# Optimization experiments

Measured on AMD Instinct MI355X. Metric: run time of the kernel, lower is better.

The kernel has to match this reference:

```python
import jax, jax.numpy as jnp
from jax import lax
import numpy as np

NBINS = 50

def _make_filters():
    coords = np.linspace(-1.0, 1.0, 3)
    zz, yy, xx = np.meshgrid(coords, coords, coords, indexing='ij')
    gf = []
    for freq in [2.0, 4.0]:
        for ang in [0.0, np.pi / 4, np.pi / 2, 3 * np.pi / 4]:
            gauss = np.exp(-(xx ** 2 + yy ** 2 + zz ** 2) / 0.5)
            f = gauss * np.cos(freq * (xx * np.cos(ang) + yy * np.sin(ang)))
            f = f - f.mean()
            s = f.std(ddof=1)  # torch std is unbiased
            if s > 1e-8:
                f = f / s
            gf.append(f)
    gf = np.stack(gf)[:, None].astype(np.float32)  # (8,1,3,3,3)
    lf = []
    for axis in range(3):
        for sign in [1, -1]:
            f = np.zeros((3, 3, 3), np.float32)
            f[1, 1, 1] = 1.0
            idx = [1, 1, 1]
            idx[axis] += sign
            f[tuple(idx)] = -1.0
            lf.append(f)
    lf = np.stack(lf)[:, None].astype(np.float32)  # (6,1,3,3,3)
    return gf, lf

def setup_inputs() -> dict:
    key = jax.random.key(0)
    k1, k2 = jax.random.split(key)
    B, D, H, W = 4, 96, 160, 160
    x = jax.random.uniform(k1, (B, 1, D, H, W), jnp.float32, minval=-1.0, maxval=1.0)
    mask = (jax.random.uniform(k2, (B, 1, D, H, W), jnp.float32) > 0.5).astype(jnp.float32)
    gf, lf = _make_filters()
    return {"x": x, "mask": mask, "gabor_filters": jnp.asarray(gf), "lbp_filters": jnp.asarray(lf)}

def _hu_stats(v, mf):
    # v, mf: (B,D,H,W); mf is 0/1 float mask
    n = mf.sum((1, 2, 3))                      # (B,)
    nn = jnp.maximum(n, 1.0)
    mu = (mf * v).sum((1, 2, 3)) / nn
    diff = (v - mu[:, None, None, None]) * mf
    var = (diff ** 2).sum((1, 2, 3)) / jnp.maximum(n - 1.0, 1.0)  # unbiased, like torch .std()
    sigma = jnp.sqrt(var) + 1e-8
    z = diff / sigma[:, None, None, None]
    skew = (z ** 3).sum((1, 2, 3)) / nn
    kurt = (z ** 4).sum((1, 2, 3)) / nn - 3.0
    # histogram over [-1,1] with 50 bins; torch.histc ignores out-of-range, last bin inclusive
    w = mf * ((v >= -1.0) & (v <= 1.0)).astype(v.dtype)
    idx = jnp.clip(jnp.floor((v + 1.0) * (NBINS / 2.0)).astype(jnp.int32), 0, NBINS - 1)
    hist = jax.vmap(lambda i, wb: jnp.zeros((NBINS,), v.dtype).at[i.ravel()].add(wb.ravel()))(idx, w)
    p = hist / (hist.sum(-1, keepdims=True) + 1e-8)
    ent = -(p * jnp.log(p + 1e-8)).sum(-1)
    valid = (n >= 10.0).astype(v.dtype)
    return jnp.stack([mu, sigma, skew, kurt, ent], axis=1) * valid[:, None]  # (B,5)

def _glcm_proxy(v, m):
    # v: (B,D,H,W) float; m: (B,D,H,W) bool
    rows = []
    for axis in range(3):
        a = axis + 1
        sl1 = tuple(slice(None, -1) if i == a else slice(None) for i in range(4))
        sl2 = tuple(slice(1, None) if i == a else slice(None) for i in range(4))
        d = v[sl1] - v[sl2]
        mp = (m[sl1] & m[sl2]).astype(v.dtype)
        s = mp.sum((1, 2, 3))
        ss = jnp.maximum(s, 1.0)
        con = (mp * d * d).sum((1, 2, 3)) / ss
        hom = (mp / (1.0 + d * d)).sum((1, 2, 3)) / ss
        ok = (s >= 4.0).astype(v.dtype)
        rows += [con * ok, hom * ok]
    return jnp.stack(rows, axis=1)  # (B,6)

def _forward(x, mask, gabor_filters, lbp_filters):
    v = x[:, 0]                       # (B,D,H,W)
    m = mask[:, 0] > 0.5              # bool
    mf = m.astype(x.dtype)
    hu = _hu_stats(v, mf)             # (B,5)
    dn = ('NCDHW', 'OIDHW', 'NCDHW')
    pad = [(1, 1)] * 3
    gab = lax.conv_general_dilated(x, gabor_filters, (1, 1, 1), pad, dimension_numbers=dn)
    lung_vol = jnp.clip(mask.sum((2, 3, 4)), 1.0, None)      # (B,1)
    gab_feat = jnp.abs(gab * mask).sum((2, 3, 4)) / lung_vol  # (B,8)
    lbp = lax.conv_general_dilated(x, lbp_filters, (1, 1, 1), pad, dimension_numbers=dn)
    lbp = lbp * mask
    lbp_feat = ((lbp > 0).astype(x.dtype) * mask).sum((2, 3, 4)) / lung_vol  # (B,6)
    glcm = _glcm_proxy(v, m)          # (B,6)
    return jnp.concatenate([hu, gab_feat, lbp_feat, glcm], axis=1)  # (B,25)

def reference(x, mask, gabor_filters, lbp_filters):
    return _forward(x, mask, gabor_filters, lbp_filters)
```

## Files before the change

kernel.cpp:

```cpp
#include <hip/hip_runtime.h>
#include <math.h>

#define B_    4
#define D_    96
#define H_    160
#define W_    160
#define HW_   (H_ * W_)
#define NVOX  (D_ * H_ * W_)
#define NBINS 50
#define NQR   28
#define CPB   256
#define PART_F (B_ * NQR * CPB)
#define HIST_U PART_F
#define WQ_F   (PART_F + 200)
#define LASTP ((D_ - 1) * HW_)

typedef float f2 __attribute__((ext_vector_type(2)));

__device__ __forceinline__ float rfl(float v) {
    return __uint_as_float(__builtin_amdgcn_readfirstlane(__float_as_uint(v)));
}

__global__ __launch_bounds__(64) void radiomics_weights(
    const float* __restrict__ gf, const float* __restrict__ lf,
    float* __restrict__ ws)
{
    const int lane = threadIdx.x;
    __shared__ float sCs[8][5], sR[8], sMO[8], sMC[8];
    if (lane < 8) {
        const int f = lane;
        float O9[9], C9[9];
        float mC = 0.f, mO = 0.f;
#pragma unroll
        for (int k = 0; k < 9; ++k) {
            O9[k] = gf[f * 27 + k];
            C9[k] = gf[f * 27 + 9 + k];
            mC += C9[k]; mO += O9[k];
        }
        mC *= (1.f / 9.f); mO *= (1.f / 9.f);
        float cov = 0.f, var = 0.f;
#pragma unroll
        for (int k = 0; k < 9; ++k) {
            float c = C9[k] - mC, o = O9[k] - mO;
            cov += c * o; var += c * c;
        }
        sR[f] = cov / var; sMO[f] = mO; sMC[f] = mC;
#pragma unroll
        for (int j = 0; j < 4; ++j) sCs[f][j] = 0.5f * (C9[j] + C9[8 - j]);
        sCs[f][4] = C9[4];
    }
    __syncthreads();
    if (lane == 0) {
        float* wq = ws + WQ_F;
        float gz0 = 0.f;
        for (int f = 0; f < 8; ++f) gz0 += sR[f];
        gz0 *= 0.125f;
        wq[0] = gz0;
        float df[8];
        for (int f = 0; f < 8; ++f) df[f] = sMO[f] - gz0 * sMC[f];
        for (int F = 0; F < 2; ++F) {
            const int f0 = 4 * F, f1 = 4 * F + 1, f2 = 4 * F + 2, f3 = 4 * F + 3;
            float* g = wq + 1 + 11 * F;
            g[0]  = 0.5f * (df[f0] + df[f2]);
            g[1]  = 0.5f * (sCs[f0][0] + sCs[f2][0]);
            g[2]  = 0.5f * (sCs[f0][2] + sCs[f2][2]);
            g[3]  = 0.5f * (sCs[f0][4] + sCs[f2][4]);
            g[4]  = 0.5f * (sCs[f0][1] + sCs[f2][3]);
            g[5]  = 0.5f * (sCs[f0][3] + sCs[f2][1]);
            g[6]  = 0.5f * (df[f1] + df[f3]);
            g[7]  = 0.25f * (sCs[f1][1] + sCs[f1][3]
                           + sCs[f3][1] + sCs[f3][3]);
            g[8]  = 0.5f * (sCs[f1][4] + sCs[f3][4]);
            g[9]  = 0.5f * (sCs[f1][0] + sCs[f3][2]);
            g[10] = 0.5f * (sCs[f1][2] + sCs[f3][0]);
        }
    }
    unsigned int* gh = (unsigned int*)ws + HIST_U;
    for (int i = lane; i < B_ * NBINS; i += 64) gh[i] = 0u;
}

#define LOADP(s, zo) do {                                                   \
    _Pragma("unroll")                                                       \
    for (int r_ = 0; r_ < 3; ++r_) {                                        \
        Xw[s][r_][0] = xbb[(zo) + rowoff[r_] + xL];                         \
        f2 t_ = *(const f2*)(xbb + (zo) + rowoff[r_] + gx);                 \
        Xw[s][r_][1] = t_.x; Xw[s][r_][2] = t_.y;                           \
        Xw[s][r_][3] = xbb[(zo) + rowoff[r_] + xR];                         \
    }                                                                       \
} while (0)

#define FINISH(s, bzv) do {                                                 \
    if ((bzv) == 0.f) {                                                     \
        _Pragma("unroll")                                                   \
        for (int r_ = 0; r_ < 3; ++r_)                                      \
            _Pragma("unroll")                                               \
            for (int c_ = 0; c_ < 4; ++c_) Xw[s][r_][c_] = 0.f;             \
        S9[s][0] = S9[s][1] = 0.f;                                          \
    } else {                                                                \
        _Pragma("unroll")                                                   \
        for (int c_ = 0; c_ < 4; ++c_) {                                    \
            Xw[s][0][c_] *= bndRow0; Xw[s][2][c_] *= bndRow2;               \
        }                                                                   \
        _Pragma("unroll")                                                   \
        for (int r_ = 0; r_ < 3; ++r_) {                                    \
            Xw[s][r_][0] *= bndL; Xw[s][r_][3] *= bndR;                     \
        }                                                                   \
        float cs0_ = Xw[s][0][0] + Xw[s][1][0] + Xw[s][2][0];               \
        float cs1_ = Xw[s][0][1] + Xw[s][1][1] + Xw[s][2][1];               \
        float cs2_ = Xw[s][0][2] + Xw[s][1][2] + Xw[s][2][2];               \
        float cs3_ = Xw[s][0][3] + Xw[s][1][3] + Xw[s][2][3];               \
        S9[s][0] = cs0_ + cs1_ + cs2_;                                      \
        S9[s][1] = cs1_ + cs2_ + cs3_;                                      \
    }                                                                       \
} while (0)

__global__ __launch_bounds__(256) void radiomics_main(
    const float* __restrict__ x, const float* __restrict__ mask,
    float* __restrict__ ws)
{
    __shared__ unsigned int shist[4 * NBINS];
    __shared__ float xred[4][NQR];

    const int tid = threadIdx.x;
    const int tx = tid & 15, ty = tid >> 4;
    const int lane = tid & 63, wid = tid >> 6;

    for (int i = tid; i < 4 * NBINS; i += 256) shist[i] = 0u;

    const float* wq = ws + WQ_F;
    const float gz0 = rfl(wq[0]);
    float gco[22];
#pragma unroll
    for (int i = 0; i < 22; ++i) gco[i] = rfl(wq[1 + i]);

    const int c = blockIdx.x;
    const int b = blockIdx.z;
    int t, z0, nz;
    if (c < 36) {
        t  = c / 6;
        const int ci = c - 6 * t;
        z0 = 16 * ci; nz = 16;
    } else {
        const int c2i = c - 36;
        const int ti = c2i / 5;
        const int ci = c2i - 5 * ti;
        t = 6 + ti;
        if (ci == 0) { z0 = 0; nz = 16; }
        else         { z0 = 20 * ci - 4; nz = 20; }
    }
    const int ngroups = nz >> 2;

    const int gx = (t % 5) * 32 + tx * 2;
    const int gy = (t / 5) * 16 + ty;

    const float* __restrict__ xbb = x    + (size_t)b * NVOX;
    const float* __restrict__ mbb = mask + (size_t)b * NVOX;

    const int gy0 = (gy > 0) ? gy - 1 : 0;
    const int gy2 = (gy + 1 < H_) ? gy + 1 : H_ - 1;
    const int rowoff[3] = { gy0 * W_, gy * W_, gy2 * W_ };
    const float bndRow0 = (gy > 0) ? 1.f : 0.f;
    const float bndRow2 = (gy + 1 < H_) ? 1.f : 0.f;
    const int xL = (gx > 0) ? gx - 1 : 0;
    const int xR = (gx + 2 < W_) ? gx + 2 : W_ - 1;
    const float bndL = (gx > 0) ? 1.f : 0.f;
    const float bndR = (gx + 2 < W_) ? 1.f : 0.f;
    const int moff  = gy * W_ + gx;
    const int myoff = gy2 * W_ + gx;
    const int mxoff = gy * W_ + xR;
    const float bym = bndRow2, bxm = bndR;

    float Xw[4][3][4];
    float S9[4][2];
    float Mq[4][2];
    float bzs[4];
    f2    myq[2];
    float mxq[2];
    float acc[NQR];
#pragma unroll
    for (int q = 0; q < NQR; ++q) acc[q] = 0.f;
    bzs[0] = bzs[1] = bzs[2] = 1.f;

    if (z0 == 0) {
#pragma unroll
        for (int r = 0; r < 3; ++r)
#pragma unroll
            for (int cc = 0; cc < 4; ++cc) Xw[0][r][cc] = 0.f;
        S9[0][0] = S9[0][1] = 0.f;
    } else {
        LOADP(0, (z0 - 1) * HW_);
        FINISH(0, 1.f);
    }
    LOADP(1, z0 * HW_);
    FINISH(1, 1.f);
    {
        f2 mm = *(const f2*)(mbb + z0 * HW_ + moff);
        Mq[1][0] = (mm.x > 0.5f) ? 1.f : 0.f;
        Mq[1][1] = (mm.y > 0.5f) ? 1.f : 0.f;
    }
    LOADP(2, (z0 + 1) * HW_);
    {
        f2 mm = *(const f2*)(mbb + (z0 + 1) * HW_ + moff);
        Mq[2][0] = mm.x; Mq[2][1] = mm.y;
    }
    Mq[0][0] = Mq[0][1] = 0.f;
    myq[0] = *(const f2*)(mbb + z0 * HW_ + myoff);
    mxq[0] = mbb[z0 * HW_ + mxoff];

    int zc   = z0 * HW_;
    int zpre = (z0 + 2) * HW_;

#pragma unroll 1
    for (int g = 0; g < ngroups; ++g) {
#pragma unroll
        for (int j = 0; j < 4; ++j) {
            const int c0 = j & 3;
            const int cs = (j + 1) & 3;
            const int c2 = (j + 2) & 3;
            const int c3 = (j + 3) & 3;
            const int cur = j & 1, nxt = cur ^ 1;

            const int zpe = (zpre < NVOX) ? zpre : LASTP;
            bzs[c3] = (zpre < NVOX) ? 1.f : 0.f;
            LOADP(c3, zpe);
            {
                f2 mm = *(const f2*)(mbb + zpe + moff);
                Mq[c3][0] = mm.x; Mq[c3][1] = mm.y;
            }
            const int zn = (zc + HW_ < NVOX) ? zc + HW_ : LASTP;
            myq[nxt] = *(const f2*)(mbb + zn + myoff);
            mxq[nxt] = mbb[zn + mxoff];

            const f2 my2 = myq[cur];
            const float mxs = mxq[cur];

#pragma unroll
            for (int q = 0; q < 2; ++q) {
                const float v  = Xw[cs][1][q + 1];
                const float mc = Mq[cs][q];

                acc[0] += mc;
                float mv  = mc * v;  acc[1] += mv;
                float mv2 = mv * v;  acc[2] += mv2;
                float mv3 = mv2 * v; acc[3] += mv3;
                acc[4] += mv3 * v;

                if (mc > 0.5f && v >= -1.f && v <= 1.f) {
                    int bi = (int)((v + 1.f) * (NBINS * 0.5f));
                    bi = min(bi, NBINS - 1);
                    atomicAdd(&shist[(tid >> 6) * NBINS + bi], 1u);
                }

                acc[14] += (v > Xw[c0][1][q + 1]) ? mc : 0.f;
                acc[15] += (v > Xw[cs][2][q + 1]) ? mc : 0.f;
                acc[16] += (v > Xw[cs][0][q + 1]) ? mc : 0.f;
                acc[17] += (v > Xw[cs][1][q + 2]) ? mc : 0.f;
                acc[18] += (v > Xw[cs][1][q])     ? mc : 0.f;

                {
                    float mr = (q == 0) ? my2.x : my2.y;
                    float mp = mc * (((mr > 0.5f) ? 1.f : 0.f) * bym);
                    float d = v - Xw[cs][2][q + 1], dd = d * d;
                    acc[20] += mp;
                    acc[23] = fmaf(mp, dd, acc[23]);
                    acc[26] = fmaf(mp, __builtin_amdgcn_rcpf(1.f + dd), acc[26]);
                }
                {
                    float mnr = (q == 0) ? Mq[cs][1] : (((mxs > 0.5f) ? 1.f : 0.f) * bxm);
                    float mp = mc * mnr;
                    float d = v - Xw[cs][1][q + 2], dd = d * d;
                    acc[21] += mp;
                    acc[24] = fmaf(mp, dd, acc[24]);
                    acc[27] = fmaf(mp, __builtin_amdgcn_rcpf(1.f + dd), acc[27]);
                }
            }

            FINISH(c2, bzs[c2]);
            Mq[c2][0] = (Mq[c2][0] * bzs[c2] > 0.5f) ? 1.f : 0.f;
            Mq[c2][1] = (Mq[c2][1] * bzs[c2] > 0.5f) ? 1.f : 0.f;

            float T6[3][4];
#pragma unroll
            for (int r = 0; r < 3; ++r)
#pragma unroll
                for (int cc = 0; cc < 4; ++cc)
                    T6[r][cc] = fmaf(gz0, Xw[c0][r][cc] + Xw[c2][r][cc], Xw[cs][r][cc]);

#pragma unroll
            for (int q = 0; q < 2; ++q) {
                const float v  = Xw[cs][1][q + 1];
                const float mc = Mq[cs][q];

                float P0 = T6[0][q]     + T6[2][q + 2];
                float P1 = T6[0][q + 1] + T6[2][q + 1];
                float P2 = T6[0][q + 2] + T6[2][q];
                float P3 = T6[1][q]     + T6[1][q + 2];
                float ctrv = T6[1][q + 1];
                float S2 = S9[c0][q] + S9[c2][q];
                float Qv = P1 + P3;
#pragma unroll
                for (int F = 0; F < 2; ++F) {
                    const float dfA = gco[F*11+0], c0s = gco[F*11+1];
                    const float c2s = gco[F*11+2], c4s = gco[F*11+3];
                    const float cu  = gco[F*11+4], cw  = gco[F*11+5];
                    const float dfB = gco[F*11+6], ct  = gco[F*11+7];
                    const float ce  = gco[F*11+8], ca  = gco[F*11+9];
                    const float cb  = gco[F*11+10];
                    float E = dfA * S2;
                    E = fmaf(c0s, P0, E); E = fmaf(c2s, P2, E); E = fmaf(c4s, ctrv, E);
                    float r0   = fmaf(cu, P1, fmaf(cw, P3, E));
                    float r90  = fmaf(cw, P1, fmaf(cu, P3, E));
                    float G = fmaf(ct, Qv, dfB * S2);
                    G = fmaf(ce, ctrv, G);
                    float r45  = fmaf(ca, P0, fmaf(cb, P2, G));
                    float r135 = fmaf(cb, P0, fmaf(ca, P2, G));
                    acc[5 + 4*F + 0] = fmaf(fabsf(r0),   mc, acc[5 + 4*F + 0]);
                    acc[5 + 4*F + 1] = fmaf(fabsf(r45),  mc, acc[5 + 4*F + 1]);
                    acc[5 + 4*F + 2] = fmaf(fabsf(r90),  mc, acc[5 + 4*F + 2]);
                    acc[5 + 4*F + 3] = fmaf(fabsf(r135), mc, acc[5 + 4*F + 3]);
                }

                acc[13] += (v > Xw[c2][1][q + 1]) ? mc : 0.f;

                {
                    float mp = mc * Mq[c2][q];
                    float d = v - Xw[c2][1][q + 1], dd = d * d;
                    acc[19] += mp;
                    acc[22] = fmaf(mp, dd, acc[22]);
                    acc[25] = fmaf(mp, __builtin_amdgcn_rcpf(1.f + dd), acc[25]);
                }
            }
            zc += HW_; zpre += HW_;
        }
    }

#pragma unroll
    for (int q = 0; q < NQR; ++q) {
        float sm = acc[q];
#pragma unroll
        for (int o = 32; o > 0; o >>= 1)
            sm += __shfl_down(sm, o, 64);
        acc[q] = sm;
    }
    if (lane == 0) {
#pragma unroll
        for (int q = 0; q < NQR; ++q) xred[wid][q] = acc[q];
    }
    __syncthreads();

    if (tid < NQR) {
        float v = xred[0][tid] + xred[1][tid] + xred[2][tid] + xred[3][tid];
        ws[((size_t)b * NQR + tid) * CPB + c] = v;
    } else if (tid < NQR + NBINS) {
        int h = tid - NQR;
        unsigned int cnt = shist[h] + shist[NBINS + h]
                         + shist[2 * NBINS + h] + shist[3 * NBINS + h];
        unsigned int* ghist = (unsigned int*)ws + HIST_U;
        if (cnt) atomicAdd(&ghist[b * NBINS + h], cnt);
    }
}

__global__ __launch_bounds__(512) void radiomics_tail(
    const float* __restrict__ ws, float* __restrict__ out)
{
    __shared__ double fin[NQR];
    __shared__ double hcnt[NBINS];
    __shared__ double entp[NBINS];
    __shared__ double sh_hsum;
    const int b = blockIdx.x, tid = threadIdx.x;
    const int wave = tid >> 6, lane = tid & 63;

    for (int q = wave; q < NQR; q += 8) {
        const float* p = ws + ((size_t)b * NQR + q) * CPB;
        double s = 0.0;
#pragma unroll
        for (int k = 0; k < 4; ++k)
            s += (double)p[lane + 64 * k];
#pragma unroll
        for (int o = 32; o > 0; o >>= 1)
            s += __shfl_down(s, o, 64);
        if (lane == 0) fin[q] = s;
    }
    if (tid < NBINS)
        hcnt[tid] = (double)(((const unsigned int*)ws)[HIST_U + b * NBINS + tid]);
    __syncthreads();

    if (tid == 0) {
        double h = 0.0;
        for (int k = 0; k < NBINS; ++k) h += hcnt[k];
        sh_hsum = h + 1e-8;
    }
    __syncthreads();

    if (tid < NBINS) {
        double p = hcnt[tid] / sh_hsum;
        entp[tid] = -p * log(p + 1e-8);
    }
    __syncthreads();

    if (tid == 0) {
        const double n  = fin[0];
        const double nn = fmax(n, 1.0);
        const double s1 = fin[1], s2 = fin[2], s3 = fin[3], s4 = fin[4];
        const double mu = s1 / nn;
        const double M2 = s2 - 2.0 * mu * s1 + mu * mu * n;
        const double M3 = s3 - 3.0 * mu * s2 + 3.0 * mu * mu * s1 - mu * mu * mu * n;
        const double M4 = s4 - 4.0 * mu * s3 + 6.0 * mu * mu * s2
                          - 4.0 * mu * mu * mu * s1 + mu * mu * mu * mu * n;
        const double var   = M2 / fmax(n - 1.0, 1.0);
        const double sigma = sqrt(var) + 1e-8;
        const double skew  = M3 / (sigma * sigma * sigma) / nn;
        const double kurt  = M4 / (sigma * sigma * sigma * sigma) / nn - 3.0;

        double ent = 0.0;
        for (int k = 0; k < NBINS; ++k) ent += entp[k];

        const double valid = (n >= 10.0) ? 1.0 : 0.0;
        float* ob = out + b * 25;
        ob[0] = (float)(mu * valid);
        ob[1] = (float)(sigma * valid);
        ob[2] = (float)(skew * valid);
        ob[3] = (float)(kurt * valid);
        ob[4] = (float)(ent * valid);

        const double lung = fmax(n, 1.0);
        for (int f = 0; f < 8; ++f) ob[5 + f]  = (float)(fin[5 + f] / lung);
        for (int f = 0; f < 6; ++f) ob[13 + f] = (float)(fin[13 + f] / lung);

        for (int ax = 0; ax < 3; ++ax) {
            double s  = fin[19 + ax];
            double ss = fmax(s, 1.0);
            double ok = (s >= 4.0) ? 1.0 : 0.0;
            ob[19 + 2 * ax]     = (float)(fin[22 + ax] / ss * ok);
            ob[19 + 2 * ax + 1] = (float)(fin[25 + ax] / ss * ok);
        }
    }
}

extern "C" void kernel_launch(void* const* d_in, const int* in_sizes, int n_in,
                              void* d_out, int out_size, void* d_ws, size_t ws_size,
                              hipStream_t stream)
{
    const float* x    = (const float*)d_in[0];
    const float* mask = (const float*)d_in[1];
    const float* gf   = (const float*)d_in[2];
    const float* lf   = (const float*)d_in[3];
    float* out = (float*)d_out;
    float* ws  = (float*)d_ws;

    radiomics_weights<<<1, 64, 0, stream>>>(gf, lf, ws);
    radiomics_main<<<dim3(256, 1, B_), 256, 0, stream>>>(x, mask, ws);
    radiomics_tail<<<B_, 512, 0, stream>>>(ws, out);
}
```

Baseline: 165.4 us.

## Share y-neighbour rows via wave shuffles and rebalance z-chunk partition

Each thread now loads only its centre row plus one halo row (top row in a wave for the upper halo, bottom row for the lower), and gets the other y-neighbours from adjacent lanes with __shfl_up/__shfl_down by 16. This cuts global loads per slice from three rows to two and shrinks register arrays. The z-slicing is also redone so the grid has 320 blocks per batch with a different chunk split, and the tail reduction is widened to match. The cost is extra shuffle instructions and select logic.

```diff
diff --git a/kernel.cpp b/kernel.cpp
--- a/kernel.cpp
+++ b/kernel.cpp
@@ -9,7 +9,7 @@
 #define NVOX  (D_ * H_ * W_)
 #define NBINS 50
 #define NQR   28
-#define CPB   256
+#define CPB   320
 #define PART_F (B_ * NQR * CPB)
 #define HIST_U PART_F
 #define WQ_F   (PART_F + 200)
@@ -79,38 +79,35 @@
     for (int i = lane; i < B_ * NBINS; i += 64) gh[i] = 0u;
 }
 
-#define LOADP(s, zo) do {                                                   \
-    _Pragma("unroll")                                                       \
-    for (int r_ = 0; r_ < 3; ++r_) {                                        \
-        Xw[s][r_][0] = xbb[(zo) + rowoff[r_] + xL];                         \
-        f2 t_ = *(const f2*)(xbb + (zo) + rowoff[r_] + gx);                 \
-        Xw[s][r_][1] = t_.x; Xw[s][r_][2] = t_.y;                           \
-        Xw[s][r_][3] = xbb[(zo) + rowoff[r_] + xR];                         \
-    }                                                                       \
+#define LOADR(s, zo) do {                                                   \
+    Xc[s][0] = xbb[(zo) + rowC + xL];                                       \
+    f2 t_ = *(const f2*)(xbb + (zo) + rowC + gx);                           \
+    Xc[s][1] = t_.x; Xc[s][2] = t_.y;                                       \
+    Xc[s][3] = xbb[(zo) + rowC + xR];                                       \
+    hal[s][0] = xbb[(zo) + rowH + xL];                                      \
+    f2 h_ = *(const f2*)(xbb + (zo) + rowH + gx);                           \
+    hal[s][1] = h_.x; hal[s][2] = h_.y;                                     \
+    hal[s][3] = xbb[(zo) + rowH + xR];                                      \
 } while (0)
 
 #define FINISH(s, bzv) do {                                                 \
     if ((bzv) == 0.f) {                                                     \
-        _Pragma("unroll")                                                   \
-        for (int r_ = 0; r_ < 3; ++r_)                                      \
-            _Pragma("unroll")                                               \
-            for (int c_ = 0; c_ < 4; ++c_) Xw[s][r_][c_] = 0.f;             \
+        Xc[s][0] = Xc[s][1] = Xc[s][2] = Xc[s][3] = 0.f;                    \
+        hal[s][0] = hal[s][1] = hal[s][2] = hal[s][3] = 0.f;                \
         S9[s][0] = S9[s][1] = 0.f;                                          \
     } else {                                                                \
-        _Pragma("unroll")                                                   \
-        for (int c_ = 0; c_ < 4; ++c_) {                                    \
-            Xw[s][0][c_] *= bndRow0; Xw[s][2][c_] *= bndRow2;               \
-        }                                                                   \
-        _Pragma("unroll")                                                   \
-        for (int r_ = 0; r_ < 3; ++r_) {                                    \
-            Xw[s][r_][0] *= bndL; Xw[s][r_][3] *= bndR;                     \
-        }                                                                   \
-        float cs0_ = Xw[s][0][0] + Xw[s][1][0] + Xw[s][2][0];               \
-        float cs1_ = Xw[s][0][1] + Xw[s][1][1] + Xw[s][2][1];               \
-        float cs2_ = Xw[s][0][2] + Xw[s][1][2] + Xw[s][2][2];               \
-        float cs3_ = Xw[s][0][3] + Xw[s][1][3] + Xw[s][2][3];               \
-        S9[s][0] = cs0_ + cs1_ + cs2_;                                      \
-        S9[s][1] = cs1_ + cs2_ + cs3_;                                      \
+        Xc[s][0] *= bndL; Xc[s][3] *= bndR;                                 \
+        hal[s][0] *= bndL; hal[s][3] *= bndR;                               \
+        float rs0_ = Xc[s][0] + Xc[s][1] + Xc[s][2];                        \
+        float rs1_ = Xc[s][1] + Xc[s][2] + Xc[s][3];                        \
+        float hrs0_ = hal[s][0] + hal[s][1] + hal[s][2];                    \
+        float hrs1_ = hal[s][1] + hal[s][2] + hal[s][3];                    \
+        float u0_ = __shfl_up(rs0_, 16, 64), d0_ = __shfl_down(rs0_, 16, 64); \
+        float u1_ = __shfl_up(rs1_, 16, 64), d1_ = __shfl_down(rs1_, 16, 64); \
+        S9[s][0] = (isTop ? hrs0_ : u0_) * bndRow0 + rs0_                   \
+                 + (isBot ? hrs0_ : d0_) * bndRow2;                         \
+        S9[s][1] = (isTop ? hrs1_ : u1_) * bndRow0 + rs1_                   \
+                 + (isBot ? hrs1_ : d1_) * bndRow2;                         \
     }                                                                       \
 } while (0)
 
@@ -123,7 +120,10 @@
 
     const int tid = threadIdx.x;
     const int tx = tid & 15, ty = tid >> 4;
+    const int tyw = ty & 3;
     const int lane = tid & 63, wid = tid >> 6;
+    const bool isTop = (tyw == 0);
+    const bool isBot = (tyw == 3);
 
     for (int i = tid; i < 4 * NBINS; i += 256) shist[i] = 0u;
 
@@ -136,17 +136,17 @@
     const int c = blockIdx.x;
     const int b = blockIdx.z;
     int t, z0, nz;
-    if (c < 36) {
-        t  = c / 6;
-        const int ci = c - 6 * t;
+    if (c < 140) {
+        t = c / 7;
+        const int ci = c - 7 * t;
+        if (ci < 3) { z0 = 16 * ci; nz = 16; }
+        else        { z0 = 48 + 12 * (ci - 3); nz = 12; }
+    } else {
+        const int c2i = c - 140;
+        const int ti = c2i / 6;
+        const int ci = c2i - 6 * ti;
+        t = 20 + ti;
         z0 = 16 * ci; nz = 16;
-    } else {
-        const int c2i = c - 36;
-        const int ti = c2i / 5;
-        const int ci = c2i - 5 * ti;
-        t = 6 + ti;
-        if (ci == 0) { z0 = 0; nz = 16; }
-        else         { z0 = 20 * ci - 4; nz = 20; }
     }
     const int ngroups = nz >> 2;
 
@@ -158,7 +158,8 @@
 
     const int gy0 = (gy > 0) ? gy - 1 : 0;
     const int gy2 = (gy + 1 < H_) ? gy + 1 : H_ - 1;
-    const int rowoff[3] = { gy0 * W_, gy * W_, gy2 * W_ };
+    const int rowC = gy * W_;
+    const int rowH = (isBot ? gy2 : gy0) * W_;
     const float bndRow0 = (gy > 0) ? 1.f : 0.f;
     const float bndRow2 = (gy + 1 < H_) ? 1.f : 0.f;
     const int xL = (gx > 0) ? gx - 1 : 0;
@@ -170,35 +171,32 @@
     const int mxoff = gy * W_ + xR;
     const float bym = bndRow2, bxm = bndR;
 
-    float Xw[4][3][4];
+    float Xc[4][4];
+    float hal[4][4];
     float S9[4][2];
     float Mq[4][2];
-    float bzs[4];
     f2    myq[2];
     float mxq[2];
     float acc[NQR];
 #pragma unroll
     for (int q = 0; q < NQR; ++q) acc[q] = 0.f;
-    bzs[0] = bzs[1] = bzs[2] = 1.f;
 
     if (z0 == 0) {
 #pragma unroll
-        for (int r = 0; r < 3; ++r)
-#pragma unroll
-            for (int cc = 0; cc < 4; ++cc) Xw[0][r][cc] = 0.f;
+        for (int cc = 0; cc < 4; ++cc) { Xc[0][cc] = 0.f; hal[0][cc] = 0.f; }
         S9[0][0] = S9[0][1] = 0.f;
     } else {
-        LOADP(0, (z0 - 1) * HW_);
+        LOADR(0, (z0 - 1) * HW_);
         FINISH(0, 1.f);
     }
-    LOADP(1, z0 * HW_);
+    LOADR(1, z0 * HW_);
     FINISH(1, 1.f);
     {
         f2 mm = *(const f2*)(mbb + z0 * HW_ + moff);
         Mq[1][0] = (mm.x > 0.5f) ? 1.f : 0.f;
         Mq[1][1] = (mm.y > 0.5f) ? 1.f : 0.f;
     }
-    LOADP(2, (z0 + 1) * HW_);
+    LOADR(2, (z0 + 1) * HW_);
     {
         f2 mm = *(const f2*)(mbb + (z0 + 1) * HW_ + moff);
         Mq[2][0] = mm.x; Mq[2][1] = mm.y;
@@ -207,6 +205,7 @@
     myq[0] = *(const f2*)(mbb + z0 * HW_ + myoff);
     mxq[0] = mbb[z0 * HW_ + mxoff];
 
+    int z    = z0;
     int zc   = z0 * HW_;
     int zpre = (z0 + 2) * HW_;
 
@@ -221,8 +220,7 @@
             const int cur = j & 1, nxt = cur ^ 1;
 
             const int zpe = (zpre < NVOX) ? zpre : LASTP;
-            bzs[c3] = (zpre < NVOX) ? 1.f : 0.f;
-            LOADP(c3, zpe);
+            LOADR(c3, zpe);
             {
                 f2 mm = *(const f2*)(mbb + zpe + moff);
                 Mq[c3][0] = mm.x; Mq[c3][1] = mm.y;
@@ -234,9 +232,18 @@
             const f2 my2 = myq[cur];
             const float mxs = mxq[cur];
 
+            float yup[2], ydn[2];
 #pragma unroll
             for (int q = 0; q < 2; ++q) {
-                const float v  = Xw[cs][1][q + 1];
+                float up = __shfl_up(Xc[cs][q + 1], 16, 64);
+                float dn = __shfl_down(Xc[cs][q + 1], 16, 64);
+                yup[q] = (isTop ? hal[cs][q + 1] : up) * bndRow0;
+                ydn[q] = (isBot ? hal[cs][q + 1] : dn) * bndRow2;
+            }
+
+#pragma unroll
+            for (int q = 0; q < 2; ++q) {
+                const float v  = Xc[cs][q + 1];
                 const float mc = Mq[cs][q];
 
                 acc[0] += mc;
@@ -251,16 +258,16 @@
                     atomicAdd(&shist[(tid >> 6) * NBINS + bi], 1u);
                 }
 
-                acc[14] += (v > Xw[c0][1][q + 1]) ? mc : 0.f;
-                acc[15] += (v > Xw[cs][2][q + 1]) ? mc : 0.f;
-                acc[16] += (v > Xw[cs][0][q + 1]) ? mc : 0.f;
-                acc[17] += (v > Xw[cs][1][q + 2]) ? mc : 0.f;
-                acc[18] += (v > Xw[cs][1][q])     ? mc : 0.f;
+                acc[14] += (v > Xc[c0][q + 1]) ? mc : 0.f;
+                acc[15] += (v > ydn[q])        ? mc : 0.f;
+                acc[16] += (v > yup[q])        ? mc : 0.f;
+                acc[17] += (v > Xc[cs][q + 2]) ? mc : 0.f;
+                acc[18] += (v > Xc[cs][q])     ? mc : 0.f;
 
                 {
                     float mr = (q == 0) ? my2.x : my2.y;
                     float mp = mc * (((mr > 0.5f) ? 1.f : 0.f) * bym);
-                    float d = v - Xw[cs][2][q + 1], dd = d * d;
+                    float d = v - ydn[q], dd = d * d;
                     acc[20] += mp;
                     acc[23] = fmaf(mp, dd, acc[23]);
                     acc[26] = fmaf(mp, __builtin_amdgcn_rcpf(1.f + dd), acc[26]);
@@ -268,34 +275,39 @@
                 {
                     float mnr = (q == 0) ? Mq[cs][1] : (((mxs > 0.5f) ? 1.f : 0.f) * bxm);
                     float mp = mc * mnr;
-                    float d = v - Xw[cs][1][q + 2], dd = d * d;
+                    float d = v - Xc[cs][q + 2], dd = d * d;
                     acc[21] += mp;
                     acc[24] = fmaf(mp, dd, acc[24]);
                     acc[27] = fmaf(mp, __builtin_amdgcn_rcpf(1.f + dd), acc[27]);
                 }
             }
 
-            FINISH(c2, bzs[c2]);
-            Mq[c2][0] = (Mq[c2][0] * bzs[c2] > 0.5f) ? 1.f : 0.f;
-            Mq[c2][1] = (Mq[c2][1] * bzs[c2] > 0.5f) ? 1.f : 0.f;
-
-            float T6[3][4];
-#pragma unroll
-            for (int r = 0; r < 3; ++r)
-#pragma unroll
-                for (int cc = 0; cc < 4; ++cc)
-                    T6[r][cc] = fmaf(gz0, Xw[c0][r][cc] + Xw[c2][r][cc], Xw[cs][r][cc]);
+            const float bzn = (z + 1 < D_) ? 1.f : 0.f;
+            FINISH(c2, bzn);
+            Mq[c2][0] = (Mq[c2][0] * bzn > 0.5f) ? 1.f : 0.f;
+            Mq[c2][1] = (Mq[c2][1] * bzn > 0.5f) ? 1.f : 0.f;
+
+            float T6c[4], T6u[4], T6d[4];
+#pragma unroll
+            for (int cc = 0; cc < 4; ++cc) {
+                T6c[cc] = fmaf(gz0, Xc[c0][cc] + Xc[c2][cc], Xc[cs][cc]);
+                float th = fmaf(gz0, hal[c0][cc] + hal[c2][cc], hal[cs][cc]);
+                float up = __shfl_up(T6c[cc], 16, 64);
+                float dn = __shfl_down(T6c[cc], 16, 64);
+                T6u[cc] = (isTop ? th : up) * bndRow0;
+                T6d[cc] = (isBot ? th : dn) * bndRow2;
+            }
 
 #pragma unroll
             for (int q = 0; q < 2; ++q) {
-                const float v  = Xw[cs][1][q + 1];
+                const float v  = Xc[cs][q + 1];
                 const float mc = Mq[cs][q];
 
-                float P0 = T6[0][q]     + T6[2][q + 2];
-                float P1 = T6[0][q + 1] + T6[2][q + 1];
-                float P2 = T6[0][q + 2] + T6[2][q];
-                float P3 = T6[1][q]     + T6[1][q + 2];
-                float ctrv = T6[1][q + 1];
+                float P0 = T6u[q]     + T6d[q + 2];
+                float P1 = T6u[q + 1] + T6d[q + 1];
+                float P2 = T6u[q + 2] + T6d[q];
+                float P3 = T6c[q]     + T6c[q + 2];
+                float ctrv = T6c[q + 1];
                 float S2 = S9[c0][q] + S9[c2][q];
                 float Qv = P1 + P3;
 #pragma unroll
@@ -320,17 +332,17 @@
                     acc[5 + 4*F + 3] = fmaf(fabsf(r135), mc, acc[5 + 4*F + 3]);
                 }
 
-                acc[13] += (v > Xw[c2][1][q + 1]) ? mc : 0.f;
+                acc[13] += (v > Xc[c2][q + 1]) ? mc : 0.f;
 
                 {
                     float mp = mc * Mq[c2][q];
-                    float d = v - Xw[c2][1][q + 1], dd = d * d;
+                    float d = v - Xc[c2][q + 1], dd = d * d;
                     acc[19] += mp;
                     acc[22] = fmaf(mp, dd, acc[22]);
                     acc[25] = fmaf(mp, __builtin_amdgcn_rcpf(1.f + dd), acc[25]);
                 }
             }
-            zc += HW_; zpre += HW_;
+            ++z; zc += HW_; zpre += HW_;
         }
     }
 
@@ -374,7 +386,7 @@
         const float* p = ws + ((size_t)b * NQR + q) * CPB;
         double s = 0.0;
 #pragma unroll
-        for (int k = 0; k < 4; ++k)
+        for (int k = 0; k < 5; ++k)
             s += (double)p[lane + 64 * k];
 #pragma unroll
         for (int o = 32; o > 0; o >>= 1)
@@ -449,6 +461,6 @@
     float* ws  = (float*)d_ws;
 
     radiomics_weights<<<1, 64, 0, stream>>>(gf, lf, ws);
-    radiomics_main<<<dim3(256, 1, B_), 256, 0, stream>>>(x, mask, ws);
+    radiomics_main<<<dim3(CPB, 1, B_), 256, 0, stream>>>(x, mask, ws);
     radiomics_tail<<<B_, 512, 0, stream>>>(ws, out);
 }
```

Result: no change. 162.5 us (-1.7%).
